# Performance work log

Hardware: AMD Instinct MI355X
Metric: run time of the kernel (lower is better)

## Reference

```python
import jax, jax.numpy as jnp
import numpy as np

GROUP_SIZE = 256
QMAX = 7.0   # int4 symmetric: clamp to [-8, 7], scale from max_abs/7
QMIN = -8.0
EPS = 1e-9


def _dequantized_weight(weight):
    """Symmetric int4 group quantization (group_size=256 along input dim),
    then dequantize. Matches group_quantize_tensor_symmetric + qc4w matmul math.
    weight: [out, in] float32."""
    O, I = weight.shape
    wg = weight.reshape(O, I // GROUP_SIZE, GROUP_SIZE)
    scale = jnp.maximum(jnp.max(jnp.abs(wg), axis=-1, keepdims=True) / QMAX, EPS)
    w_int = jnp.clip(jnp.round(wg / scale), QMIN, QMAX)
    return (w_int * scale).reshape(O, I)


def setup_inputs() -> dict:
    key = jax.random.key(0)
    k1, k2 = jax.random.split(key)
    x = jax.random.normal(k1, (1, 16, 4096), dtype=jnp.float32)
    weight = jax.random.normal(k2, (14336, 4096), dtype=jnp.float32) * 0.02
    return {"x": x, "weight": weight}


def reference(x, weight):
    # x: [1, S, I]; weight: [O, I]
    w_dq = _dequantized_weight(weight)           # [O, I]
    xs = x[0]                                    # squeeze batch (asserted == 1)
    out = jnp.einsum('si,oi->so', xs, w_dq)     # [S, O]
    return out[None, ...]                        # [1, S, O]
```

## Files before the change

kernel.cpp:

```cpp
#include <hip/hip_runtime.h>


constexpr int O_DIM  = 14336;
constexpr int I_DIM  = 4096;
constexpr int S_DIM  = 16;
constexpr int GS     = 256;
constexpr int NG     = I_DIM / GS;
constexpr int RPW    = 4;
constexpr int NWAVE  = 7;
constexpr int NTHR   = 64 * NWAVE;
constexpr int RPB    = RPW * NWAVE;
constexpr int PH_I   = 1024;
constexpr int NPH    = I_DIM / PH_I;
constexpr int GPP    = PH_I / GS;

__device__ __forceinline__ float wave_max_dpp(float x) {
    int v = __float_as_int(x);
    int t;
    t = __builtin_amdgcn_update_dpp(0, v, 0x111, 0xf, 0xf, true);
    v = __float_as_int(fmaxf(__int_as_float(v), __int_as_float(t)));
    t = __builtin_amdgcn_update_dpp(0, v, 0x112, 0xf, 0xf, true);
    v = __float_as_int(fmaxf(__int_as_float(v), __int_as_float(t)));
    t = __builtin_amdgcn_update_dpp(0, v, 0x114, 0xf, 0xf, true);
    v = __float_as_int(fmaxf(__int_as_float(v), __int_as_float(t)));
    t = __builtin_amdgcn_update_dpp(0, v, 0x118, 0xf, 0xf, true);
    v = __float_as_int(fmaxf(__int_as_float(v), __int_as_float(t)));
    t = __builtin_amdgcn_update_dpp(0, v, 0x142, 0xf, 0xf, true);
    v = __float_as_int(fmaxf(__int_as_float(v), __int_as_float(t)));
    t = __builtin_amdgcn_update_dpp(0, v, 0x143, 0xf, 0xf, true);
    v = __float_as_int(fmaxf(__int_as_float(v), __int_as_float(t)));
    return __int_as_float(__builtin_amdgcn_readlane(v, 63));
}

__global__ __launch_bounds__(NTHR)
void qlin_kernel(const float* __restrict__ x,
                 const float* __restrict__ w,
                 float* __restrict__ out)
{
    __shared__ float xs[S_DIM][PH_I];

    const int tid  = threadIdx.x;
    const int lane = tid & 63;
    const int wv   = tid >> 6;
    const int row0 = blockIdx.x * RPB + wv * RPW;

    const float* wp = w + (size_t)row0 * I_DIM + lane * 4;

    float acc[RPW][S_DIM];
#pragma unroll
    for (int r = 0; r < RPW; ++r)
#pragma unroll
        for (int s = 0; s < S_DIM; ++s) acc[r][s] = 0.0f;

    float4 wcur[RPW], wnext[RPW];
#pragma unroll
    for (int r = 0; r < RPW; ++r)
        wcur[r] = *reinterpret_cast<const float4*>(wp + (size_t)r * I_DIM);

    for (int p = 0; p < NPH; ++p) {
        if (p) __syncthreads();
        for (int j = tid; j < S_DIM * (PH_I / 4); j += NTHR) {
            const int s  = j >> 8;
            const int i4 = (j & 255) * 4;
            *reinterpret_cast<float4*>(&xs[s][i4]) =
                *reinterpret_cast<const float4*>(
                    &x[(size_t)s * I_DIM + p * PH_I + i4]);
        }
        __syncthreads();

        for (int g = 0; g < GPP; ++g) {
            const int G = p * GPP + g;

            if (G + 1 < NG) {
#pragma unroll
                for (int r = 0; r < RPW; ++r)
                    wnext[r] = *reinterpret_cast<const float4*>(
                        wp + (size_t)r * I_DIM + (G + 1) * GS);
            }

#pragma unroll
            for (int r = 0; r < RPW; ++r) {
                float4 v = wcur[r];
                float m = fmaxf(fmaxf(fabsf(v.x), fabsf(v.y)),
                                fmaxf(fabsf(v.z), fabsf(v.w)));
                m = wave_max_dpp(m);
                float scale = fmaxf(m * (1.0f / 7.0f), 1e-9f);
                float invs  = 1.0f / scale;
                wcur[r].x = rintf(v.x * invs) * scale;
                wcur[r].y = rintf(v.y * invs) * scale;
                wcur[r].z = rintf(v.z * invs) * scale;
                wcur[r].w = rintf(v.w * invs) * scale;
            }

            const int xb = g * GS + lane * 4;
#pragma unroll
            for (int s = 0; s < S_DIM; ++s) {
                float4 xv = *reinterpret_cast<const float4*>(&xs[s][xb]);
#pragma unroll
                for (int r = 0; r < RPW; ++r) {
                    acc[r][s] = fmaf(wcur[r].x, xv.x, acc[r][s]);
                    acc[r][s] = fmaf(wcur[r].y, xv.y, acc[r][s]);
                    acc[r][s] = fmaf(wcur[r].z, xv.z, acc[r][s]);
                    acc[r][s] = fmaf(wcur[r].w, xv.w, acc[r][s]);
                }
            }

#pragma unroll
            for (int r = 0; r < RPW; ++r) wcur[r] = wnext[r];
        }
    }

    float a[64];
#pragma unroll
    for (int r = 0; r < RPW; ++r)
#pragma unroll
        for (int s = 0; s < S_DIM; ++s) a[(r << 4) | s] = acc[r][s];

#pragma unroll
    for (int m = 32; m >= 1; m >>= 1) {
        const bool hi = (lane & m) != 0;
#pragma unroll
        for (int j = 0; j < m; ++j) {
            float snd  = hi ? a[j] : a[j + m];
            float rcv  = __shfl_xor(snd, m, 64);
            float kept = hi ? a[j + m] : a[j];
            a[j] = kept + rcv;
        }
    }
    {
        const int r = lane >> 4, s = lane & 15;
        out[s * O_DIM + (row0 + r)] = a[0];
    }
}

extern "C" void kernel_launch(void* const* d_in, const int* in_sizes, int n_in,
                              void* d_out, int out_size, void* d_ws, size_t ws_size,
                              hipStream_t stream) {
    const float* x = (const float*)d_in[0];
    const float* w = (const float*)d_in[1];
    float* out = (float*)d_out;
    dim3 grid(O_DIM / RPB);
    dim3 block(NTHR);
    qlin_kernel<<<grid, block, 0, stream>>>(x, w, out);
}
```

Before: 336.7 us.

## Drop shared-memory x staging and read activations directly from global memory

Removes the LDS staging of x with its block-wide barriers and instead has each lane read x float4s straight from global (L2/L1-cached) memory per group. It also drops the software prefetch of the next weight group, loading weights at the top of each iteration, and shrinks blocks from 7 to 4 waves so more, smaller blocks are launched. The aim is to eliminate barrier stalls and LDS traffic and raise the number of independent waves. In exchange it relies on cache hits for the repeated x reads and loses the explicit weight-load overlap, leaving latency hiding to the hardware.

```diff
diff --git a/kernel.cpp b/kernel.cpp
--- a/kernel.cpp
+++ b/kernel.cpp
@@ -7,12 +7,9 @@
 constexpr int GS     = 256;
 constexpr int NG     = I_DIM / GS;
 constexpr int RPW    = 4;
-constexpr int NWAVE  = 7;
+constexpr int NWAVE  = 4;
 constexpr int NTHR   = 64 * NWAVE;
 constexpr int RPB    = RPW * NWAVE;
-constexpr int PH_I   = 1024;
-constexpr int NPH    = I_DIM / PH_I;
-constexpr int GPP    = PH_I / GS;
 
 __device__ __forceinline__ float wave_max_dpp(float x) {
     int v = __float_as_int(x);
@@ -37,14 +34,13 @@
                  const float* __restrict__ w,
                  float* __restrict__ out)
 {
-    __shared__ float xs[S_DIM][PH_I];
-
     const int tid  = threadIdx.x;
     const int lane = tid & 63;
     const int wv   = tid >> 6;
     const int row0 = blockIdx.x * RPB + wv * RPW;
 
     const float* wp = w + (size_t)row0 * I_DIM + lane * 4;
+    const float* xp = x + lane * 4;
 
     float acc[RPW][S_DIM];
 #pragma unroll
@@ -52,61 +48,40 @@
 #pragma unroll
         for (int s = 0; s < S_DIM; ++s) acc[r][s] = 0.0f;
 
-    float4 wcur[RPW], wnext[RPW];
+#pragma unroll 1
+    for (int G = 0; G < NG; ++G) {
+        float4 wq[RPW];
 #pragma unroll
-    for (int r = 0; r < RPW; ++r)
-        wcur[r] = *reinterpret_cast<const float4*>(wp + (size_t)r * I_DIM);
-
-    for (int p = 0; p < NPH; ++p) {
-        if (p) __syncthreads();
-        for (int j = tid; j < S_DIM * (PH_I / 4); j += NTHR) {
-            const int s  = j >> 8;
-            const int i4 = (j & 255) * 4;
-            *reinterpret_cast<float4*>(&xs[s][i4]) =
-                *reinterpret_cast<const float4*>(
-                    &x[(size_t)s * I_DIM + p * PH_I + i4]);
-        }
-        __syncthreads();
-
-        for (int g = 0; g < GPP; ++g) {
-            const int G = p * GPP + g;
-
-            if (G + 1 < NG) {
-#pragma unroll
-                for (int r = 0; r < RPW; ++r)
-                    wnext[r] = *reinterpret_cast<const float4*>(
-                        wp + (size_t)r * I_DIM + (G + 1) * GS);
-            }
+        for (int r = 0; r < RPW; ++r)
+            wq[r] = *reinterpret_cast<const float4*>(
+                wp + (size_t)r * I_DIM + G * GS);
 
 #pragma unroll
+        for (int r = 0; r < RPW; ++r) {
+            float4 v = wq[r];
+            float m = fmaxf(fmaxf(fabsf(v.x), fabsf(v.y)),
+                            fmaxf(fabsf(v.z), fabsf(v.w)));
+            m = wave_max_dpp(m);
+            float scale = fmaxf(m * (1.0f / 7.0f), 1e-9f);
+            float invs  = 1.0f / scale;
+            wq[r].x = rintf(v.x * invs) * scale;
+            wq[r].y = rintf(v.y * invs) * scale;
+            wq[r].z = rintf(v.z * invs) * scale;
+            wq[r].w = rintf(v.w * invs) * scale;
+        }
+
+        const float* xg = xp + G * GS;
+#pragma unroll
+        for (int s = 0; s < S_DIM; ++s) {
+            float4 xv = *reinterpret_cast<const float4*>(
+                &xg[(size_t)s * I_DIM]);
+#pragma unroll
             for (int r = 0; r < RPW; ++r) {
-                float4 v = wcur[r];
-                float m = fmaxf(fmaxf(fabsf(v.x), fabsf(v.y)),
-                                fmaxf(fabsf(v.z), fabsf(v.w)));
-                m = wave_max_dpp(m);
-                float scale = fmaxf(m * (1.0f / 7.0f), 1e-9f);
-                float invs  = 1.0f / scale;
-                wcur[r].x = rintf(v.x * invs) * scale;
-                wcur[r].y = rintf(v.y * invs) * scale;
-                wcur[r].z = rintf(v.z * invs) * scale;
-                wcur[r].w = rintf(v.w * invs) * scale;
+                acc[r][s] = fmaf(wq[r].x, xv.x, acc[r][s]);
+                acc[r][s] = fmaf(wq[r].y, xv.y, acc[r][s]);
+                acc[r][s] = fmaf(wq[r].z, xv.z, acc[r][s]);
+                acc[r][s] = fmaf(wq[r].w, xv.w, acc[r][s]);
             }
-
-            const int xb = g * GS + lane * 4;
-#pragma unroll
-            for (int s = 0; s < S_DIM; ++s) {
-                float4 xv = *reinterpret_cast<const float4*>(&xs[s][xb]);
-#pragma unroll
-                for (int r = 0; r < RPW; ++r) {
-                    acc[r][s] = fmaf(wcur[r].x, xv.x, acc[r][s]);
-                    acc[r][s] = fmaf(wcur[r].y, xv.y, acc[r][s]);
-                    acc[r][s] = fmaf(wcur[r].z, xv.z, acc[r][s]);
-                    acc[r][s] = fmaf(wcur[r].w, xv.w, acc[r][s]);
-                }
-            }
-
-#pragma unroll
-            for (int r = 0; r < RPW; ++r) wcur[r] = wnext[r];
         }
     }
 
```

Result: slower. 363.9 us (+8.1%).
